# Optimization experiments

Hardware: AMD Instinct MI355X
Metric: run time of the kernel (lower is better)

## Reference

```python
import jax, jax.numpy as jnp
import numpy as np

NUM_BOXES = 512
NUM_COORDS = 200000
C = 128
MAX_SELECTED = 262144  # static pad size for the ragged output
P_INSIDE = 0.002       # expected ~204.8k selected rows < MAX_SELECTED


def setup_inputs() -> dict:
    key = jax.random.key(0)
    k1, k2, k3 = jax.random.split(key, 3)
    coords = jax.random.randint(k1, (NUM_COORDS, 4), 0, 256, dtype=jnp.int32)
    features = jax.random.normal(k2, (NUM_COORDS, C), dtype=jnp.float32)
    is_inside = jax.random.uniform(k3, (NUM_BOXES, NUM_COORDS)) < P_INSIDE
    return {"coords": coords, "features": features, "is_inside": is_inside,
            "max_selected": MAX_SELECTED}


def reference(coords, features, is_inside, max_selected):
    # Faithful to select_coords/select_features, but WITHOUT materializing the
    # dense (num_boxes, num_coords, C) expand: compute flat nonzero indices of
    # the mask directly and gather once. Output is padded to a static size
    # (padded rows zeroed) since jax requires static shapes.
    num_boxes, num_coords = is_inside.shape
    total = num_boxes * num_coords
    flat_idx = jnp.nonzero(is_inside.ravel(), size=max_selected, fill_value=total)[0]
    valid = flat_idx < total                      # [K] pad mask
    safe = jnp.where(valid, flat_idx, 0)
    box_idx = (safe // num_coords).astype(jnp.int32)   # [K]
    coord_idx = safe % num_coords                       # [K]
    # select_features: features[None].expand(...)[is_inside]
    selected_features = jnp.where(valid[:, None], features[coord_idx], 0.0)  # [K, C]
    # select_coords: cat(coords[:, :-1] gathered, box index)
    sel_xyz = coords[coord_idx, :-1]                    # [K, 3]
    ext_coords = jnp.concatenate([sel_xyz, box_idx[:, None]], axis=-1)  # [K, 4]
    extended_coordinates = jnp.where(valid[:, None], ext_coords, 0)
    return extended_coordinates, selected_features
```

## Files before the change

kernel.cpp:

```cpp
#include <hip/hip_runtime.h>


#define BS  256
#define WPT 8
#define WPB (BS*WPT)

__global__ void __launch_bounds__(BS) pack_count(
    const uint4* __restrict__ d, long long totalElems, int wordsTotal,
    unsigned* __restrict__ maskOut, int* __restrict__ counts)
{
  const int tid = threadIdx.x;
  const int wBase = blockIdx.x * WPB;
  int cnt = 0;
  #pragma unroll
  for (int k = 0; k < WPT; ++k){
    const int w = wBase + k*BS + tid;
    if (w >= wordsTotal) break;
    const long long e0 = (long long)w << 5;
    unsigned m = 0;
    if (e0 + 31 < totalElems){
      const uint4* base = d + 8*(long long)w;
      #pragma unroll
      for (int q = 0; q < 8; ++q){
        uint4 x = base[q];
        m |= ((unsigned)(x.x!=0) << (4*q))   | ((unsigned)(x.y!=0) << (4*q+1)) |
             ((unsigned)(x.z!=0) << (4*q+2)) | ((unsigned)(x.w!=0) << (4*q+3));
      }
    } else {
      const unsigned* p32 = (const unsigned*)d;
      for (int b2 = 0; b2 < 32 && e0 + b2 < totalElems; ++b2)
        if (p32[e0 + b2]) m |= (1u << b2);
    }
    maskOut[w] = m;
    cnt += __popc(m);
  }
  const int lane = tid & 63, wid = tid >> 6;
  for (int off = 32; off > 0; off >>= 1) cnt += __shfl_down(cnt, off, 64);
  __shared__ int wsum[BS/64];
  if (lane == 0) wsum[wid] = cnt;
  __syncthreads();
  if (tid == 0)
    counts[blockIdx.x] = wsum[0] + wsum[1] + wsum[2] + wsum[3];
}

__global__ void __launch_bounds__(BS) emit_kernel(
    const unsigned* __restrict__ mask, const int* __restrict__ counts,
    int wordsTotal, int numTiles, int max_sel,
    int* __restrict__ outIdx, int* __restrict__ totalOut)
{
  const int tid = threadIdx.x;
  const int lane = tid & 63, wid = tid >> 6;
  const int bid = blockIdx.x;
  __shared__ int wsum[BS/64];
  __shared__ int sh_base;

  int pre = 0;
  for (int i = tid; i < bid; i += BS) pre += counts[i];
  int red = pre;
  for (int off = 32; off > 0; off >>= 1) red += __shfl_down(red, off, 64);
  if (lane == 0) wsum[wid] = red;
  __syncthreads();
  if (tid == 0){
    const int base = wsum[0] + wsum[1] + wsum[2] + wsum[3];
    sh_base = base;
    if (bid == numTiles - 1) *totalOut = base + counts[bid];
  }
  __syncthreads();

  int running = sh_base;
  const int wBase = bid * WPB;
  #pragma unroll
  for (int it = 0; it < WPT; ++it){
    const int w = wBase + it*BS + tid;
    unsigned m = (w < wordsTotal) ? mask[w] : 0u;
    const int cnt = __popc(m);
    int incl = cnt;
    for (int off = 1; off < 64; off <<= 1){
      int t = __shfl_up(incl, off, 64);
      if (lane >= off) incl += t;
    }
    if (lane == 63) wsum[wid] = incl;
    __syncthreads();
    int wbase = 0;
    for (int ww = 0; ww < wid; ++ww) wbase += wsum[ww];
    int iterTotal = 0;
    for (int ww = 0; ww < BS/64; ++ww) iterTotal += wsum[ww];
    int pos = running + wbase + incl - cnt;
    if (m){
      const long long e0 = (long long)w << 5;
      unsigned mm = m;
      while (mm){
        const int b = __ffs(mm) - 1;
        mm &= mm - 1;
        if (pos < max_sel) outIdx[pos] = (int)(e0 + b);
        ++pos;
      }
    }
    running += iterTotal;
    __syncthreads();
  }
}

__global__ void __launch_bounds__(BS) gather_kernel(
    const int* __restrict__ selIdx, const int* __restrict__ totalPtr,
    const int4* __restrict__ coords, const float4* __restrict__ feat,
    int num_coords, int c4, int max_sel,
    float4* __restrict__ outExt, float4* __restrict__ outFeat)
{
  const int lane    = threadIdx.x & 31;
  const int g0      = (blockIdx.x*blockDim.x + threadIdx.x) >> 5;
  const int gstride = (gridDim.x*blockDim.x) >> 5;
  int total = *totalPtr;
  if (total > max_sel) total = max_sel;
  const float4 z = make_float4(0.f, 0.f, 0.f, 0.f);
  for (int r = g0; r < max_sel; r += gstride){
    float4* dst = outFeat + (long long)r*c4;
    if (r < total){
      const int flat = selIdx[r];
      const unsigned box = (unsigned)flat / (unsigned)num_coords;
      const int ci = flat - (int)box*num_coords;
      const float4* src = feat + (long long)ci*c4;
      for (int c = lane; c < c4; c += 32) dst[c] = src[c];
      if (lane == 0){
        int4 cc = coords[ci];
        outExt[r] = make_float4((float)cc.x, (float)cc.y, (float)cc.z, (float)box);
      }
    } else {
      for (int c = lane; c < c4; c += 32) dst[c] = z;
      if (lane == 0) outExt[r] = z;
    }
  }
}

extern "C" void kernel_launch(void* const* d_in, const int* in_sizes, int n_in,
                              void* d_out, int out_size, void* d_ws, size_t ws_size,
                              hipStream_t stream){
  const int*   coords   = (const int*)d_in[0];
  const float* features = (const float*)d_in[1];
  const void*  inside   = d_in[2];

  const int num_coords = in_sizes[0] / 4;
  const int C          = in_sizes[1] / num_coords;
  const int c4         = C / 4;
  const long long totalElems = (long long)in_sizes[2];
  const int max_sel    = out_size / (4 + C);

  const int wordsTotal = (int)((totalElems + 31) / 32);
  const int numTiles   = (wordsTotal + WPB - 1) / WPB;

  int* counts  = (int*)d_ws;
  int* total   = counts + numTiles;
  int* selIdx  = total + 1;
  unsigned* maskBuf = (unsigned*)(selIdx + max_sel);

  hipLaunchKernelGGL(pack_count, dim3(numTiles), dim3(BS), 0, stream,
                     (const uint4*)inside, totalElems, wordsTotal, maskBuf, counts);

  hipLaunchKernelGGL(emit_kernel, dim3(numTiles), dim3(BS), 0, stream,
                     maskBuf, counts, wordsTotal, numTiles, max_sel, selIdx, total);

  hipLaunchKernelGGL(gather_kernel, dim3(2048), dim3(BS), 0, stream,
                     selIdx, total, (const int4*)coords, (const float4*)features,
                     num_coords, c4, max_sel,
                     (float4*)d_out,
                     (float4*)((float*)d_out + (long long)max_sel*4));
}
```

Baseline: 662.7 us.

## Fuse index emission with feature gather via LDS staging and tail-zeroing blocks

```diff
diff --git a/kernel.cpp b/kernel.cpp
--- a/kernel.cpp
+++ b/kernel.cpp
@@ -1,9 +1,11 @@
 #include <hip/hip_runtime.h>
 
 
-#define BS  256
-#define WPT 8
-#define WPB (BS*WPT)
+#define BS    256
+#define WPT   8
+#define WPB   (BS*WPT)
+#define CAP   2048
+#define TAILB 256
 
 __global__ void __launch_bounds__(BS) pack_count(
     const uint4* __restrict__ d, long long totalElems, int wordsTotal,
@@ -43,16 +45,41 @@
     counts[blockIdx.x] = wsum[0] + wsum[1] + wsum[2] + wsum[3];
 }
 
-__global__ void __launch_bounds__(BS) emit_kernel(
+__global__ void __launch_bounds__(BS) emit_gather(
     const unsigned* __restrict__ mask, const int* __restrict__ counts,
     int wordsTotal, int numTiles, int max_sel,
-    int* __restrict__ outIdx, int* __restrict__ totalOut)
+    const int4* __restrict__ coords, const float4* __restrict__ feat,
+    int num_coords, int c4,
+    int* __restrict__ selOvf,
+    float4* __restrict__ outExt, float4* __restrict__ outFeat)
 {
   const int tid = threadIdx.x;
   const int lane = tid & 63, wid = tid >> 6;
   const int bid = blockIdx.x;
   __shared__ int wsum[BS/64];
   __shared__ int sh_base;
+  __shared__ int ldsFlat[CAP];
+  const int w32 = tid >> 5, l32 = tid & 31;
+
+  if (bid >= numTiles){
+    int pre = 0;
+    for (int i = tid; i < numTiles; i += BS) pre += counts[i];
+    int red = pre;
+    for (int off = 32; off > 0; off >>= 1) red += __shfl_down(red, off, 64);
+    if (lane == 0) wsum[wid] = red;
+    __syncthreads();
+    int total = wsum[0] + wsum[1] + wsum[2] + wsum[3];
+    if (total > max_sel) total = max_sel;
+    const int tailWarps = TAILB * (BS >> 5);
+    const int gw = (bid - numTiles)*(BS >> 5) + w32;
+    const float4 z = make_float4(0.f, 0.f, 0.f, 0.f);
+    for (int r = total + gw; r < max_sel; r += tailWarps){
+      float4* dst = outFeat + (long long)r*c4;
+      for (int c = l32; c < c4; c += 32) dst[c] = z;
+      if (l32 == 0) outExt[r] = z;
+    }
+    return;
+  }
 
   int pre = 0;
   for (int i = tid; i < bid; i += BS) pre += counts[i];
@@ -60,14 +87,11 @@
   for (int off = 32; off > 0; off >>= 1) red += __shfl_down(red, off, 64);
   if (lane == 0) wsum[wid] = red;
   __syncthreads();
-  if (tid == 0){
-    const int base = wsum[0] + wsum[1] + wsum[2] + wsum[3];
-    sh_base = base;
-    if (bid == numTiles - 1) *totalOut = base + counts[bid];
-  }
+  if (tid == 0) sh_base = wsum[0] + wsum[1] + wsum[2] + wsum[3];
   __syncthreads();
+  const int base = sh_base;
 
-  int running = sh_base;
+  int running = base;
   const int wBase = bid * WPB;
   #pragma unroll
   for (int it = 0; it < WPT; ++it){
@@ -81,53 +105,41 @@
     }
     if (lane == 63) wsum[wid] = incl;
     __syncthreads();
-    int wbase = 0;
-    for (int ww = 0; ww < wid; ++ww) wbase += wsum[ww];
+    int wbase2 = 0;
+    for (int ww = 0; ww < wid; ++ww) wbase2 += wsum[ww];
     int iterTotal = 0;
     for (int ww = 0; ww < BS/64; ++ww) iterTotal += wsum[ww];
-    int pos = running + wbase + incl - cnt;
+    int pos = running + wbase2 + incl - cnt;
     if (m){
       const long long e0 = (long long)w << 5;
       unsigned mm = m;
       while (mm){
         const int b = __ffs(mm) - 1;
         mm &= mm - 1;
-        if (pos < max_sel) outIdx[pos] = (int)(e0 + b);
+        const int slot = pos - base;
+        if (slot < CAP) ldsFlat[slot] = (int)(e0 + b);
+        else if (pos < max_sel) selOvf[pos] = (int)(e0 + b);
         ++pos;
       }
     }
     running += iterTotal;
     __syncthreads();
   }
-}
 
-__global__ void __launch_bounds__(BS) gather_kernel(
-    const int* __restrict__ selIdx, const int* __restrict__ totalPtr,
-    const int4* __restrict__ coords, const float4* __restrict__ feat,
-    int num_coords, int c4, int max_sel,
-    float4* __restrict__ outExt, float4* __restrict__ outFeat)
-{
-  const int lane    = threadIdx.x & 31;
-  const int g0      = (blockIdx.x*blockDim.x + threadIdx.x) >> 5;
-  const int gstride = (gridDim.x*blockDim.x) >> 5;
-  int total = *totalPtr;
-  if (total > max_sel) total = max_sel;
-  const float4 z = make_float4(0.f, 0.f, 0.f, 0.f);
-  for (int r = g0; r < max_sel; r += gstride){
+  const int tileCnt = running - base;
+  int nRows = max_sel - base;
+  if (nRows > tileCnt) nRows = tileCnt;
+  for (int s = w32; s < nRows; s += (BS >> 5)){
+    const int flat = (s < CAP) ? ldsFlat[s] : selOvf[base + s];
+    const int r = base + s;
+    const unsigned box = (unsigned)flat / (unsigned)num_coords;
+    const int ci = flat - (int)box*num_coords;
+    const float4* src = feat + (long long)ci*c4;
     float4* dst = outFeat + (long long)r*c4;
-    if (r < total){
-      const int flat = selIdx[r];
-      const unsigned box = (unsigned)flat / (unsigned)num_coords;
-      const int ci = flat - (int)box*num_coords;
-      const float4* src = feat + (long long)ci*c4;
-      for (int c = lane; c < c4; c += 32) dst[c] = src[c];
-      if (lane == 0){
-        int4 cc = coords[ci];
-        outExt[r] = make_float4((float)cc.x, (float)cc.y, (float)cc.z, (float)box);
-      }
-    } else {
-      for (int c = lane; c < c4; c += 32) dst[c] = z;
-      if (lane == 0) outExt[r] = z;
+    for (int c = l32; c < c4; c += 32) dst[c] = src[c];
+    if (l32 == 0){
+      int4 cc = coords[ci];
+      outExt[r] = make_float4((float)cc.x, (float)cc.y, (float)cc.z, (float)box);
     }
   }
 }
@@ -149,19 +161,16 @@
   const int numTiles   = (wordsTotal + WPB - 1) / WPB;
 
   int* counts  = (int*)d_ws;
-  int* total   = counts + numTiles;
-  int* selIdx  = total + 1;
-  unsigned* maskBuf = (unsigned*)(selIdx + max_sel);
+  int* selOvf  = counts + numTiles;
+  unsigned* maskBuf = (unsigned*)(selOvf + max_sel);
 
   hipLaunchKernelGGL(pack_count, dim3(numTiles), dim3(BS), 0, stream,
                      (const uint4*)inside, totalElems, wordsTotal, maskBuf, counts);
 
-  hipLaunchKernelGGL(emit_kernel, dim3(numTiles), dim3(BS), 0, stream,
-                     maskBuf, counts, wordsTotal, numTiles, max_sel, selIdx, total);
-
-  hipLaunchKernelGGL(gather_kernel, dim3(2048), dim3(BS), 0, stream,
-                     selIdx, total, (const int4*)coords, (const float4*)features,
-                     num_coords, c4, max_sel,
+  hipLaunchKernelGGL(emit_gather, dim3(numTiles + TAILB), dim3(BS), 0, stream,
+                     maskBuf, counts, wordsTotal, numTiles, max_sel,
+                     (const int4*)coords, (const float4*)features,
+                     num_coords, c4, selOvf,
                      (float4*)d_out,
                      (float4*)((float*)d_out + (long long)max_sel*4));
 }
```

After: 662.7 us. About the same (-0.0%).
